# Kernel tuning notes

Measured on AMD Instinct MI355X. Metric: run time of the kernel, lower is better.

The kernel has to match this reference:

```python
import jax, jax.numpy as jnp
import numpy as np

N, D_IN, D_OUT = 128, 512, 512
B = 256

def setup_inputs() -> dict:
    key = jax.random.key(0)
    kx, kw, kb = jax.random.split(key, 3)
    x = jax.random.normal(kx, (B, N, D_IN), dtype=jnp.float32)
    # nn.Linear default init: uniform(-1/sqrt(d_in), 1/sqrt(d_in)) for weight and bias
    bound = 1.0 / np.sqrt(D_IN)
    weight = jax.random.uniform(kw, (N, D_IN, D_OUT), dtype=jnp.float32, minval=-bound, maxval=bound)
    bias = jax.random.uniform(kb, (N, D_OUT), dtype=jnp.float32, minval=-bound, maxval=bound)
    return {"x": x, "weight": weight, "bias": bias}

def reference(x, weight, bias):
    # per-position linear: out[b,n,o] = sum_i x[b,n,i] * W[n,i,o] + bias[n,o]
    out = jnp.einsum('bni,nio->bno', x, weight)
    return out + bias[None]
```

## Files before the change

kernel.cpp:

```cpp
#include <hip/hip_runtime.h>

typedef __attribute__((ext_vector_type(8))) __bf16 bf16x8;
typedef __attribute__((ext_vector_type(4))) float f32x4;

#define DI   512
#define DO   512
#define XROW (128 * DI)
#define OROW (128 * DO)
#define BK   32


__global__ __launch_bounds__(512, 4)
void nlinear_mfma(const float* __restrict__ xp, const float* __restrict__ wp,
                  const float* __restrict__ bp, float* __restrict__ op) {
  int blk = blockIdx.x;
  int L  = ((blk & 7) << 7) + (blk >> 3);
  int n  = L >> 3;
  int mt = (L >> 2) & 1;
  int ot = L & 3;
  int mBase = mt << 7;
  int oBase = ot << 7;

  __shared__ float  aT[128 * 32];
  __shared__ __bf16 bT[128 * 32];

  int tid  = threadIdx.x;
  int wid  = tid >> 6;
  int lane = tid & 63;
  int wm  = (wid >> 2) << 6;
  int wn  = (wid & 3) << 5;
  int l16 = lane & 15;
  int l4  = lane >> 4;

  unsigned aOff[2];
  #pragma unroll
  for (int i = 0; i < 2; ++i) {
    int r0  = (wid << 4) + (i << 3);
    int row = r0 + (lane >> 3);
    int g   = (lane & 7) ^ ((row >> 1) & 7);
    aOff[i] = (unsigned)(((mBase + row) * XROW + n * DI) * 4 + g * 16);
  }

  int bo   = (tid & 63) + (((tid >> 6) & 1) << 6);
  int bks  = (tid >> 7) & 3;
  unsigned bOff = (unsigned)((((unsigned)n * DI + (bks << 3)) * DO + oBase + bo) * 4);
  int bWslot = bks ^ ((bo >> 1) & 3);

  float bReg[8];
  auto loadB = [&](int kt) {
    #pragma unroll
    for (int r = 0; r < 8; ++r)
      bReg[r] = *(const float*)((const char*)wp + bOff + (unsigned)(kt * BK + r) * (DO * 4));
  };
  auto writeB = [&]() {
    bf16x8 v;
    #pragma unroll
    for (int r = 0; r < 8; ++r)
      v[r] = (__bf16)bReg[r];
    *(bf16x8*)((char*)bT + bo * 64 + bWslot * 16) = v;
  };

  auto gloadA = [&](int kt) {
    #pragma unroll
    for (int i = 0; i < 2; ++i) {
      int r0 = (wid << 4) + (i << 3);
      __builtin_amdgcn_global_load_lds(
          (const __attribute__((address_space(1))) void*)
              ((const char*)xp + aOff[i] + (unsigned)(kt * 128)),
          (__attribute__((address_space(3))) void*)((char*)aT + r0 * 128),
          16, 0, 0);
    }
  };

  f32x4 acc[4][2];
  #pragma unroll
  for (int i = 0; i < 4; ++i)
    #pragma unroll
    for (int j = 0; j < 2; ++j)
      acc[i][j] = f32x4{0.f, 0.f, 0.f, 0.f};

  auto compute = [&]() {
    bf16x8 bfr[2];
    #pragma unroll
    for (int j = 0; j < 2; ++j) {
      int row  = wn + j * 16 + l16;
      int slot = l4 ^ ((row >> 1) & 3);
      bfr[j] = *(const bf16x8*)((const char*)bT + row * 64 + slot * 16);
    }
    #pragma unroll
    for (int i = 0; i < 4; ++i) {
      int row = wm + i * 16 + l16;
      int v7  = (row >> 1) & 7;
      const char* rb = (const char*)aT + row * 128;
      f32x4 lo = *(const f32x4*)(rb + (((2 * l4)     ^ v7) * 16));
      f32x4 hi = *(const f32x4*)(rb + (((2 * l4 + 1) ^ v7) * 16));
      bf16x8 a;
      a[0] = (__bf16)lo.x; a[1] = (__bf16)lo.y; a[2] = (__bf16)lo.z; a[3] = (__bf16)lo.w;
      a[4] = (__bf16)hi.x; a[5] = (__bf16)hi.y; a[6] = (__bf16)hi.z; a[7] = (__bf16)hi.w;
      acc[i][0] = __builtin_amdgcn_mfma_f32_16x16x32_bf16(a, bfr[0], acc[i][0], 0, 0, 0);
      acc[i][1] = __builtin_amdgcn_mfma_f32_16x16x32_bf16(a, bfr[1], acc[i][1], 0, 0, 0);
    }
  };

  float bi[2];
  #pragma unroll
  for (int j = 0; j < 2; ++j)
    bi[j] = bp[n * DO + oBase + wn + j * 16 + l16];

  loadB(0);
  for (int kt = 0; kt < 16; ++kt) {
    __syncthreads();
    gloadA(kt);
    writeB();
    if (kt < 15) loadB(kt + 1);
    __syncthreads();
    compute();
  }

  #pragma unroll
  for (int i = 0; i < 4; ++i) {
    #pragma unroll
    for (int j = 0; j < 2; ++j) {
      #pragma unroll
      for (int r = 0; r < 4; ++r) {
        int m = mBase + wm + i * 16 + l4 * 4 + r;
        int o = oBase + wn + j * 16 + l16;
        op[(size_t)m * OROW + n * DO + o] = acc[i][j][r] + bi[j];
      }
    }
  }
}

extern "C" void kernel_launch(void* const* d_in, const int* in_sizes, int n_in,
                              void* d_out, int out_size, void* d_ws, size_t ws_size,
                              hipStream_t stream) {
  const float* x = (const float*)d_in[0];
  const float* w = (const float*)d_in[1];
  const float* b = (const float*)d_in[2];
  float* o = (float*)d_out;
  hipLaunchKernelGGL(nlinear_mfma, dim3(1024), dim3(512), 0, stream, x, w, b, o);
}
```

Before: 54.44 us.

## Double-buffer LDS tiles and prefetch two K-steps ahead with manual waitcnt

Splits the A and B shared-memory tiles into two buffers, so each K-step computes from one buffer while the other is being filled. Global-to-LDS loads for A and register loads for B are issued two iterations ahead. Explicit s_waitcnt vmcnt/lgkmcnt, raw s_barrier and sched_barrier replace the two __syncthreads per iteration, which removes a barrier and overlaps memory latency with MFMA work. In exchange, LDS use per block doubles, which may cut the number of resident blocks per CU, and correctness now depends on hand-counted vmcnt values.

```diff
diff --git a/kernel.cpp b/kernel.cpp
--- a/kernel.cpp
+++ b/kernel.cpp
@@ -8,6 +8,11 @@
 #define XROW (128 * DI)
 #define OROW (128 * DO)
 #define BK   32
+
+#define VMCNT(n) asm volatile("s_waitcnt vmcnt(" #n ")" ::: "memory")
+#define LGKM0()  asm volatile("s_waitcnt lgkmcnt(0)" ::: "memory")
+#define SBAR()   __builtin_amdgcn_s_barrier()
+#define SCHED0() __builtin_amdgcn_sched_barrier(0)
 
 
 __global__ __launch_bounds__(512, 4)
@@ -21,8 +26,8 @@
   int mBase = mt << 7;
   int oBase = ot << 7;
 
-  __shared__ float  aT[128 * 32];
-  __shared__ __bf16 bT[128 * 32];
+  __shared__ float  aT[2][128 * BK];
+  __shared__ __bf16 bT[2][128 * BK];
 
   int tid  = threadIdx.x;
   int wid  = tid >> 6;
@@ -52,22 +57,21 @@
     for (int r = 0; r < 8; ++r)
       bReg[r] = *(const float*)((const char*)wp + bOff + (unsigned)(kt * BK + r) * (DO * 4));
   };
-  auto writeB = [&]() {
+  auto writeB = [&](int buf) {
     bf16x8 v;
     #pragma unroll
     for (int r = 0; r < 8; ++r)
       v[r] = (__bf16)bReg[r];
-    *(bf16x8*)((char*)bT + bo * 64 + bWslot * 16) = v;
+    *(bf16x8*)((char*)bT[buf] + bo * 64 + bWslot * 16) = v;
   };
-
-  auto gloadA = [&](int kt) {
+  auto gloadA = [&](int buf, int kt) {
     #pragma unroll
     for (int i = 0; i < 2; ++i) {
       int r0 = (wid << 4) + (i << 3);
       __builtin_amdgcn_global_load_lds(
           (const __attribute__((address_space(1))) void*)
               ((const char*)xp + aOff[i] + (unsigned)(kt * 128)),
-          (__attribute__((address_space(3))) void*)((char*)aT + r0 * 128),
+          (__attribute__((address_space(3))) void*)((char*)aT[buf] + r0 * 128),
           16, 0, 0);
     }
   };
@@ -79,19 +83,19 @@
     for (int j = 0; j < 2; ++j)
       acc[i][j] = f32x4{0.f, 0.f, 0.f, 0.f};
 
-  auto compute = [&]() {
+  auto compute = [&](int buf) {
     bf16x8 bfr[2];
     #pragma unroll
     for (int j = 0; j < 2; ++j) {
       int row  = wn + j * 16 + l16;
       int slot = l4 ^ ((row >> 1) & 3);
-      bfr[j] = *(const bf16x8*)((const char*)bT + row * 64 + slot * 16);
+      bfr[j] = *(const bf16x8*)((const char*)bT[buf] + row * 64 + slot * 16);
     }
     #pragma unroll
     for (int i = 0; i < 4; ++i) {
       int row = wm + i * 16 + l16;
       int v7  = (row >> 1) & 7;
-      const char* rb = (const char*)aT + row * 128;
+      const char* rb = (const char*)aT[buf] + row * 128;
       f32x4 lo = *(const f32x4*)(rb + (((2 * l4)     ^ v7) * 16));
       f32x4 hi = *(const f32x4*)(rb + (((2 * l4 + 1) ^ v7) * 16));
       bf16x8 a;
@@ -108,13 +112,36 @@
     bi[j] = bp[n * DO + oBase + wn + j * 16 + l16];
 
   loadB(0);
+  gloadA(0, 0);
+  writeB(0);
+  loadB(1);
+  gloadA(1, 1);
+  SCHED0();
+  VMCNT(10);
+  LGKM0();
+  SBAR();
+  SCHED0();
+
   for (int kt = 0; kt < 16; ++kt) {
-    __syncthreads();
-    gloadA(kt);
-    writeB();
-    if (kt < 15) loadB(kt + 1);
-    __syncthreads();
-    compute();
+    int cur = kt & 1;
+    compute(cur);
+    if (kt < 15) {
+      SBAR();
+      SCHED0();
+      writeB(cur ^ 1);
+      if (kt < 14) {
+        loadB(kt + 2);
+        gloadA(cur, kt + 2);
+        SCHED0();
+        VMCNT(10);
+      } else {
+        SCHED0();
+        VMCNT(0);
+      }
+      LGKM0();
+      SBAR();
+      SCHED0();
+    }
   }
 
   #pragma unroll
```

New measurement: 53.82 us. About the same (-1.1%).

## Triple-buffer LDS with explicit vmcnt waits and a single barrier per k-step

Applied to the files above, without the earlier changes.

Replaces the two-barrier single-buffer loop with a three-stage LDS ring: A tiles are prefetched two steps ahead via global_load_lds, and W is prefetched three steps ahead into alternating register sets before being written as bf16. Each step waits on explicit vmcnt/lgkmcnt counts and one s_barrier, so global loads overlap the MFMA compute. LDS per block grows to 72KB dynamic, which may cut the resident blocks per CU below the launch-bounds target, and the hand-tuned vmcnt values depend on the compiler's instruction ordering.

```diff
diff --git a/kernel.cpp b/kernel.cpp
--- a/kernel.cpp
+++ b/kernel.cpp
@@ -3,73 +3,67 @@
 typedef __attribute__((ext_vector_type(8))) __bf16 bf16x8;
 typedef __attribute__((ext_vector_type(4))) float f32x4;
 
-#define DI   512
-#define DO   512
+#define DI 512
+#define DO 512
 #define XROW (128 * DI)
 #define OROW (128 * DO)
-#define BK   32
+#define BK 32
+#define BUFSZ 24576
+#define BOFF  16384
 
+#define VMCNT(n) asm volatile("s_waitcnt vmcnt(" #n ")" ::: "memory")
+#define LGKM0()  asm volatile("s_waitcnt lgkmcnt(0)" ::: "memory")
+#define SBAR()   __builtin_amdgcn_s_barrier()
+#define SCHED0() __builtin_amdgcn_sched_barrier(0)
 
 __global__ __launch_bounds__(512, 4)
 void nlinear_mfma(const float* __restrict__ xp, const float* __restrict__ wp,
                   const float* __restrict__ bp, float* __restrict__ op) {
   int blk = blockIdx.x;
-  int L  = ((blk & 7) << 7) + (blk >> 3);
-  int n  = L >> 3;
-  int mt = (L >> 2) & 1;
-  int ot = L & 3;
-  int mBase = mt << 7;
-  int oBase = ot << 7;
+  int L = ((blk & 7) << 7) + (blk >> 3);
+  int n = L >> 3, mt = (L >> 2) & 1, ot = L & 3;
+  int mBase = mt << 7, oBase = ot << 7;
 
-  __shared__ float  aT[128 * 32];
-  __shared__ __bf16 bT[128 * 32];
+  extern __shared__ char lds[];
 
-  int tid  = threadIdx.x;
-  int wid  = tid >> 6;
-  int lane = tid & 63;
-  int wm  = (wid >> 2) << 6;
-  int wn  = (wid & 3) << 5;
-  int l16 = lane & 15;
-  int l4  = lane >> 4;
+  int tid = threadIdx.x, lane = tid & 63, wid = tid >> 6;
+  int wm = (wid >> 2) << 6, wn = (wid & 3) << 5;
+  int l16 = lane & 15, l4 = lane >> 4;
 
   unsigned aOff[2];
   #pragma unroll
   for (int i = 0; i < 2; ++i) {
-    int r0  = (wid << 4) + (i << 3);
+    int r0 = (wid << 4) + (i << 3);
     int row = r0 + (lane >> 3);
-    int g   = (lane & 7) ^ ((row >> 1) & 7);
+    int g = (lane & 7) ^ ((row >> 1) & 7);
     aOff[i] = (unsigned)(((mBase + row) * XROW + n * DI) * 4 + g * 16);
   }
 
-  int bo   = (tid & 63) + (((tid >> 6) & 1) << 6);
-  int bks  = (tid >> 7) & 3;
-  unsigned bOff = (unsigned)((((unsigned)n * DI + (bks << 3)) * DO + oBase + bo) * 4);
-  int bWslot = bks ^ ((bo >> 1) & 3);
+  int bo = tid & 127, bkq = tid >> 7;
+  const float* bSrc = wp + ((size_t)n * DI + (bkq << 3)) * DO + oBase + bo;
+  int bWrByte = BOFF + bo * 64 + ((bkq ^ ((bo >> 1) & 3)) << 4);
 
-  float bReg[8];
-  auto loadB = [&](int kt) {
-    #pragma unroll
-    for (int r = 0; r < 8; ++r)
-      bReg[r] = *(const float*)((const char*)wp + bOff + (unsigned)(kt * BK + r) * (DO * 4));
-  };
-  auto writeB = [&]() {
-    bf16x8 v;
-    #pragma unroll
-    for (int r = 0; r < 8; ++r)
-      v[r] = (__bf16)bReg[r];
-    *(bf16x8*)((char*)bT + bo * 64 + bWslot * 16) = v;
-  };
-
-  auto gloadA = [&](int kt) {
+  auto gloadA = [&](int bufOff, int kt) {
     #pragma unroll
     for (int i = 0; i < 2; ++i) {
       int r0 = (wid << 4) + (i << 3);
       __builtin_amdgcn_global_load_lds(
           (const __attribute__((address_space(1))) void*)
               ((const char*)xp + aOff[i] + (unsigned)(kt * 128)),
-          (__attribute__((address_space(3))) void*)((char*)aT + r0 * 128),
+          (__attribute__((address_space(3))) void*)(lds + bufOff + r0 * 128),
           16, 0, 0);
     }
+  };
+  auto loadB = [&](int kt, float (&r)[8]) {
+    #pragma unroll
+    for (int j = 0; j < 8; ++j)
+      r[j] = bSrc[(size_t)(kt * BK + j) * DO];
+  };
+  auto writeB = [&](int bufOff, float (&r)[8]) {
+    bf16x8 v;
+    #pragma unroll
+    for (int j = 0; j < 8; ++j) v[j] = (__bf16)r[j];
+    *(bf16x8*)(lds + bufOff + bWrByte) = v;
   };
 
   f32x4 acc[4][2];
@@ -79,21 +73,21 @@
     for (int j = 0; j < 2; ++j)
       acc[i][j] = f32x4{0.f, 0.f, 0.f, 0.f};
 
-  auto compute = [&]() {
+  auto compute = [&](int bufOff) {
     bf16x8 bfr[2];
     #pragma unroll
     for (int j = 0; j < 2; ++j) {
-      int row  = wn + j * 16 + l16;
+      int row = wn + j * 16 + l16;
       int slot = l4 ^ ((row >> 1) & 3);
-      bfr[j] = *(const bf16x8*)((const char*)bT + row * 64 + slot * 16);
+      bfr[j] = *(const bf16x8*)(lds + bufOff + BOFF + row * 64 + slot * 16);
     }
     #pragma unroll
     for (int i = 0; i < 4; ++i) {
       int row = wm + i * 16 + l16;
-      int v7  = (row >> 1) & 7;
-      const char* rb = (const char*)aT + row * 128;
-      f32x4 lo = *(const f32x4*)(rb + (((2 * l4)     ^ v7) * 16));
-      f32x4 hi = *(const f32x4*)(rb + (((2 * l4 + 1) ^ v7) * 16));
+      int v7 = (row >> 1) & 7;
+      const char* rb = lds + bufOff + row * 128;
+      f32x4 lo = *(const f32x4*)(rb + (((2 * l4) ^ v7) << 4));
+      f32x4 hi = *(const f32x4*)(rb + (((2 * l4 + 1) ^ v7) << 4));
       bf16x8 a;
       a[0] = (__bf16)lo.x; a[1] = (__bf16)lo.y; a[2] = (__bf16)lo.z; a[3] = (__bf16)lo.w;
       a[4] = (__bf16)hi.x; a[5] = (__bf16)hi.y; a[6] = (__bf16)hi.z; a[7] = (__bf16)hi.w;
@@ -107,15 +101,43 @@
   for (int j = 0; j < 2; ++j)
     bi[j] = bp[n * DO + oBase + wn + j * 16 + l16];
 
-  loadB(0);
-  for (int kt = 0; kt < 16; ++kt) {
-    __syncthreads();
-    gloadA(kt);
-    writeB();
-    if (kt < 15) loadB(kt + 1);
-    __syncthreads();
-    compute();
+  float bR0[8], bR1[8];
+  int cOff = 0, wOff = BUFSZ, gOff = 2 * BUFSZ;
+
+  gloadA(0, 0);
+  loadB(0, bR0);
+  writeB(0, bR0);
+  loadB(1, bR1);
+  gloadA(BUFSZ, 1);
+  loadB(2, bR0);
+  SCHED0();
+  LGKM0();
+  SBAR();
+  SCHED0();
+
+  #define STEP(KT, BRS, VMLINE, DO_LB, DO_GA)                     \
+    {                                                             \
+      writeB(wOff, BRS);                                          \
+      if (DO_GA) gloadA(gOff, (KT) + 2);                          \
+      if (DO_LB) loadB((KT) + 3, BRS);                            \
+      compute(cOff);                                              \
+      SCHED0();                                                   \
+      VMLINE;                                                     \
+      LGKM0();                                                    \
+      SBAR();                                                     \
+      SCHED0();                                                   \
+      int _t = cOff; cOff = wOff; wOff = gOff; gOff = _t;         \
+    }
+
+  for (int kt = 0; kt < 12; kt += 2) {
+    STEP(kt,     bR1, VMCNT(18), true, true);
+    STEP(kt + 1, bR0, VMCNT(18), true, true);
   }
+  STEP(12, bR1, VMCNT(18), true,  true);
+  STEP(13, bR0, VMCNT(2),  false, true);
+  STEP(14, bR1, VMCNT(0),  false, false);
+  compute(cOff);
+  #undef STEP
 
   #pragma unroll
   for (int i = 0; i < 4; ++i) {
@@ -138,5 +160,6 @@
   const float* w = (const float*)d_in[1];
   const float* b = (const float*)d_in[2];
   float* o = (float*)d_out;
-  hipLaunchKernelGGL(nlinear_mfma, dim3(1024), dim3(512), 0, stream, x, w, b, o);
+  hipLaunchKernelGGL(nlinear_mfma, dim3(1024), dim3(512), 3 * BUFSZ, stream,
+                     x, w, b, o);
 }
```

Result: faster. 48.41 us (-11.1%).
